# Kernel optimization log

Measured on AMD Instinct MI355X. Metric: run time of the kernel, lower is better.

## Reference

```python
import jax, jax.numpy as jnp
import numpy as np

N_NODES = 100000
N_EDGES = 1600000
N_GRAPHS = 256
NODE_F = 92
EDGE_F = 41
HID = 64


def setup_inputs() -> dict:
    key = jax.random.key(0)
    ks = jax.random.split(key, 16)
    Z = 2 * HID + EDGE_F  # 169, concat dim for CGConv
    inp = {
        "x": jax.random.normal(ks[0], (N_NODES, NODE_F), dtype=jnp.float32),
        "edge_index": jax.random.randint(ks[1], (2, N_EDGES), 0, N_NODES, dtype=jnp.int64),
        "edge_attr": jax.random.uniform(ks[2], (N_EDGES, EDGE_F), dtype=jnp.float32),
        "batch": jnp.sort(jax.random.randint(ks[3], (N_NODES,), 0, N_GRAPHS, dtype=jnp.int64)),
        # embedding Linear(node_feat_dim -> hidden)
        "emb_W": jax.random.normal(ks[4], (NODE_F, HID), dtype=jnp.float32) / np.sqrt(NODE_F),
        "emb_b": jnp.zeros((HID,), dtype=jnp.float32),
        # CGConv layer 1: gate (sigmoid) and source (softplus) linears on z=[x_i,x_j,e]
        "c1_Wf": jax.random.normal(ks[5], (Z, HID), dtype=jnp.float32) / np.sqrt(Z),
        "c1_bf": jnp.zeros((HID,), dtype=jnp.float32),
        "c1_Ws": jax.random.normal(ks[6], (Z, HID), dtype=jnp.float32) / np.sqrt(Z),
        "c1_bs": jnp.zeros((HID,), dtype=jnp.float32),
        # CGConv layer 2
        "c2_Wf": jax.random.normal(ks[7], (Z, HID), dtype=jnp.float32) / np.sqrt(Z),
        "c2_bf": jnp.zeros((HID,), dtype=jnp.float32),
        "c2_Ws": jax.random.normal(ks[8], (Z, HID), dtype=jnp.float32) / np.sqrt(Z),
        "c2_bs": jnp.zeros((HID,), dtype=jnp.float32),
        # head
        "l1_W": jax.random.normal(ks[9], (HID, 32), dtype=jnp.float32) / np.sqrt(HID),
        "l1_b": jnp.zeros((32,), dtype=jnp.float32),
        "l2_W": jax.random.normal(ks[10], (32, 2), dtype=jnp.float32) / np.sqrt(32),
        "l2_b": jnp.zeros((2,), dtype=jnp.float32),
    }
    return inp


def _cgconv(x, src, dst, edge_attr, Wf, bf, Ws, bs):
    # PyG CGConv: z = [x_i (target), x_j (source), e_ij]; msg = sigmoid(lin_f(z)) * softplus(lin_s(z))
    z = jnp.concatenate([x[dst], x[src], edge_attr], axis=-1)  # [E, 2H+D]
    msg = jax.nn.sigmoid(z @ Wf + bf) * jax.nn.softplus(z @ Ws + bs)  # [E, H]
    agg = jax.ops.segment_sum(msg, dst, num_segments=x.shape[0])  # scatter-add at targets
    return x + agg  # residual


def reference(x, edge_index, edge_attr, batch,
              emb_W, emb_b, c1_Wf, c1_bf, c1_Ws, c1_bs,
              c2_Wf, c2_bf, c2_Ws, c2_bs, l1_W, l1_b, l2_W, l2_b):
    src = edge_index[0]  # x_j
    dst = edge_index[1]  # x_i
    h = jax.nn.relu(x @ emb_W + emb_b)
    h = jax.nn.relu(_cgconv(h, src, dst, edge_attr, c1_Wf, c1_bf, c1_Ws, c1_bs))
    h = jax.nn.relu(_cgconv(h, src, dst, edge_attr, c2_Wf, c2_bf, c2_Ws, c2_bs))
    # global_mean_pool over graph ids
    sums = jax.ops.segment_sum(h, batch, num_segments=N_GRAPHS)
    cnt = jax.ops.segment_sum(jnp.ones((h.shape[0],), h.dtype), batch, num_segments=N_GRAPHS)
    pooled = sums / jnp.maximum(cnt, 1.0)[:, None]
    g = jax.nn.relu(pooled @ l1_W + l1_b)
    return g @ l2_W + l2_b  # [N_GRAPHS, 2]
```

## Files before the change

kernel.cpp:

```cpp
#include <hip/hip_runtime.h>

#define N_NODES 100000
#define N_EDGES 1600000
#define N_GRAPHS 256
#define NODE_F 92
#define EDGE_F 41
#define HID 64

typedef float f2 __attribute__((ext_vector_type(2)));
typedef float f4 __attribute__((ext_vector_type(4)));

static __device__ __forceinline__ f2 pk_fma(f2 a, f2 b, f2 c) {
    return __builtin_elementwise_fma(a, b, c);
}

__global__ __launch_bounds__(256) void k_embed(const float* __restrict__ x,
                                               const float* __restrict__ W,
                                               const float* __restrict__ b,
                                               float* __restrict__ h) {
    __shared__ float sT[23 * 256];
    for (int i = threadIdx.x; i < 23 * 256; i += 256) {
        const int kq = i >> 8, rem = i & 255, ln = rem >> 2, kk = rem & 3;
        sT[i] = W[(4 * kq + kk) * HID + ln];
    }
    __syncthreads();
    const int lane = threadIdx.x & 63;
    const int wid  = threadIdx.x >> 6;
    const int nW   = gridDim.x * 4;
    const float bias = b[lane];
    for (int n = blockIdx.x * 4 + wid; n < N_NODES; n += nW) {
        const float* xr = x + (size_t)n * NODE_F;
        float acc = bias;
#pragma unroll
        for (int k0 = 0; k0 < NODE_F; k0 += 4) {
            const f4 xv = *(const f4*)&xr[k0];
            const f4 wv = *(const f4*)&sT[(k0 >> 2) * 256 + 4 * lane];
            acc = fmaf(xv.x, wv.x, acc);
            acc = fmaf(xv.y, wv.y, acc);
            acc = fmaf(xv.z, wv.z, acc);
            acc = fmaf(xv.w, wv.w, acc);
        }
        h[(size_t)n * HID + lane] = fmaxf(acc, 0.f);
    }
}

template <int RELU_IN>
__global__ __launch_bounds__(256) void k_node_pre(const float* hin,
                                                  float* hout,
                                                  const float* __restrict__ Wf,
                                                  const float* __restrict__ Ws,
                                                  float* __restrict__ D,
                                                  float* __restrict__ S) {
    __shared__ float sW[64 * 256];
    for (int i = threadIdx.x; i < 64 * 256; i += 256) {
        const int k = i >> 8, j = i & 255, c = j >> 2, r = j & 3;
        float v;
        if (r == 0)      v = Wf[k * HID + c];
        else if (r == 1) v = Ws[k * HID + c];
        else if (r == 2) v = Wf[(64 + k) * HID + c];
        else             v = Ws[(64 + k) * HID + c];
        sW[i] = v;
    }
    __syncthreads();
    const int lane = threadIdx.x & 63;
    const int wid  = threadIdx.x >> 6;
    const int wave = blockIdx.x * 4 + wid;
    const int nW   = gridDim.x * 4;
    for (int base = wave * 8; base < N_NODES; base += nW * 8) {
        f2 accD[8] = {};
        f2 accS[8] = {};
        for (int k0 = 0; k0 < HID; k0 += 4) {
            f4 wv[4];
#pragma unroll
            for (int kk = 0; kk < 4; ++kk)
                wv[kk] = *(const f4*)&sW[(k0 + kk) * 256 + 4 * lane];
#pragma unroll
            for (int m = 0; m < 8; ++m) {
                f4 hv = *(const f4*)&hin[(size_t)(base + m) * HID + k0];
                if (RELU_IN) {
                    hv.x = fmaxf(hv.x, 0.f); hv.y = fmaxf(hv.y, 0.f);
                    hv.z = fmaxf(hv.z, 0.f); hv.w = fmaxf(hv.w, 0.f);
                }
#pragma unroll
                for (int kk = 0; kk < 4; ++kk) {
                    const f2 ev2 = {hv[kk], hv[kk]};
                    const f2 lo = __builtin_shufflevector(wv[kk], wv[kk], 0, 1);
                    const f2 hi = __builtin_shufflevector(wv[kk], wv[kk], 2, 3);
                    accD[m] = pk_fma(ev2, lo, accD[m]);
                    accS[m] = pk_fma(ev2, hi, accS[m]);
                }
            }
        }
#pragma unroll
        for (int m = 0; m < 8; ++m) {
            const size_t n = base + m;
            *(f2*)&D[n * 128 + 2 * lane] = accD[m];
            *(f2*)&S[n * 128 + 2 * lane] = accS[m];
            if (RELU_IN) hout[n * HID + lane] = fmaxf(hin[n * HID + lane], 0.f);
        }
    }
}

__global__ __launch_bounds__(256) void k_edge(const int* __restrict__ ei,
                                              const float* __restrict__ ea,
                                              const float* __restrict__ D,
                                              const float* __restrict__ S,
                                              const float* __restrict__ Wf,
                                              const float* __restrict__ Ws,
                                              const float* __restrict__ bf,
                                              const float* __restrict__ bs,
                                              float* __restrict__ agg) {
    const int lane = threadIdx.x & 63;
    f2 w[EDGE_F];
#pragma unroll
    for (int k = 0; k < EDGE_F; ++k)
        w[k] = (f2){Wf[(128 + k) * HID + lane], Ws[(128 + k) * HID + lane]};
    const f2 bias = {bf[lane], bs[lane]};
    const int wave = blockIdx.x * 4 + (threadIdx.x >> 6);
    const int nW   = gridDim.x * 4;
    for (int e0 = wave * 2; e0 < N_EDGES; e0 += nW * 2) {
        const int eA = __builtin_amdgcn_readfirstlane(e0);
        const int eB = eA + 1;
        const int srcA = __builtin_amdgcn_readfirstlane(ei[eA]);
        const int dstA = __builtin_amdgcn_readfirstlane(ei[N_EDGES + eA]);
        const int srcB = __builtin_amdgcn_readfirstlane(ei[eB]);
        const int dstB = __builtin_amdgcn_readfirstlane(ei[N_EDGES + eB]);
        const float* erA = ea + (size_t)eA * EDGE_F;
        const float* erB = ea + (size_t)eB * EDGE_F;
        f2 a0 = bias + *(const f2*)&D[(size_t)dstA * 128 + 2 * lane];
        f2 a1 = *(const f2*)&S[(size_t)srcA * 128 + 2 * lane];
        f2 b0 = bias + *(const f2*)&D[(size_t)dstB * 128 + 2 * lane];
        f2 b1 = *(const f2*)&S[(size_t)srcB * 128 + 2 * lane];
#pragma unroll
        for (int k = 0; k + 1 < EDGE_F; k += 2) {
            const float ea0 = erA[k], ea1 = erA[k + 1];
            const float eb0 = erB[k], eb1 = erB[k + 1];
            a0 = pk_fma((f2){ea0, ea0}, w[k], a0);
            b0 = pk_fma((f2){eb0, eb0}, w[k], b0);
            a1 = pk_fma((f2){ea1, ea1}, w[k + 1], a1);
            b1 = pk_fma((f2){eb1, eb1}, w[k + 1], b1);
        }
        {
            const float ea0 = erA[EDGE_F - 1], eb0 = erB[EDGE_F - 1];
            a0 = pk_fma((f2){ea0, ea0}, w[EDGE_F - 1], a0);
            b0 = pk_fma((f2){eb0, eb0}, w[EDGE_F - 1], b0);
        }
        const f2 fsA = a0 + a1;
        const f2 fsB = b0 + b1;
        const float gateA = __builtin_amdgcn_rcpf(1.f + __expf(-fsA.x));
        const float spA   = fmaxf(fsA.y, 0.f) + __logf(1.f + __expf(-fabsf(fsA.y)));
        const float gateB = __builtin_amdgcn_rcpf(1.f + __expf(-fsB.x));
        const float spB   = fmaxf(fsB.y, 0.f) + __logf(1.f + __expf(-fabsf(fsB.y)));
        unsafeAtomicAdd(&agg[(size_t)dstA * HID + lane], gateA * spA);
        unsafeAtomicAdd(&agg[(size_t)dstB * HID + lane], gateB * spB);
    }
}

__global__ __launch_bounds__(256) void k_pool(const float* __restrict__ agg,
                                              const int* __restrict__ batch,
                                              float* __restrict__ psum,
                                              float* __restrict__ pcnt) {
    const int lane = threadIdx.x & 63;
    const int wid  = threadIdx.x >> 6;
    const int wave = blockIdx.x * 4 + wid;
    const int nW   = gridDim.x * 4;
    const int chunk = (N_NODES + nW - 1) / nW;
    const int n0 = wave * chunk;
    if (n0 >= N_NODES) return;
    const int n1 = min(n0 + chunk, N_NODES);
    float acc = 0.f;
    int cur = batch[n0];
    int run = 0;
    for (int n = n0; n < n1; ++n) {
        const int g = batch[n];
        if (g != cur) {
            unsafeAtomicAdd(&psum[(size_t)cur * HID + lane], acc);
            if (lane == 0) unsafeAtomicAdd(&pcnt[cur], (float)run);
            acc = 0.f; run = 0; cur = g;
        }
        acc += fmaxf(agg[(size_t)n * HID + lane], 0.f);
        ++run;
    }
    unsafeAtomicAdd(&psum[(size_t)cur * HID + lane], acc);
    if (lane == 0) unsafeAtomicAdd(&pcnt[cur], (float)run);
}

__global__ __launch_bounds__(256) void k_head(const float* __restrict__ psum,
                                              const float* __restrict__ pcnt,
                                              const float* __restrict__ l1W,
                                              const float* __restrict__ l1b,
                                              const float* __restrict__ l2W,
                                              const float* __restrict__ l2b,
                                              float* __restrict__ out) {
    const int g = threadIdx.x;
    const float inv = 1.f / fmaxf(pcnt[g], 1.f);
    float hid[32];
#pragma unroll
    for (int j = 0; j < 32; ++j) hid[j] = l1b[j];
    for (int c = 0; c < HID; ++c) {
        const float pv = psum[(size_t)g * HID + c] * inv;
#pragma unroll
        for (int j = 0; j < 32; ++j) hid[j] = fmaf(pv, l1W[c * 32 + j], hid[j]);
    }
#pragma unroll
    for (int j = 0; j < 32; ++j) hid[j] = fmaxf(hid[j], 0.f);
#pragma unroll
    for (int k = 0; k < 2; ++k) {
        float a = l2b[k];
#pragma unroll
        for (int j = 0; j < 32; ++j) a = fmaf(hid[j], l2W[j * 2 + k], a);
        out[g * 2 + k] = a;
    }
}

extern "C" void kernel_launch(void* const* d_in, const int* in_sizes, int n_in,
                              void* d_out, int out_size, void* d_ws, size_t ws_size,
                              hipStream_t stream) {
    const float* x     = (const float*)d_in[0];
    const int*   ei    = (const int*)d_in[1];
    const float* ea    = (const float*)d_in[2];
    const int*   batch = (const int*)d_in[3];
    const float* embW  = (const float*)d_in[4];
    const float* embb  = (const float*)d_in[5];
    const float* c1Wf  = (const float*)d_in[6];
    const float* c1bf  = (const float*)d_in[7];
    const float* c1Ws  = (const float*)d_in[8];
    const float* c1bs  = (const float*)d_in[9];
    const float* c2Wf  = (const float*)d_in[10];
    const float* c2bf  = (const float*)d_in[11];
    const float* c2Ws  = (const float*)d_in[12];
    const float* c2bs  = (const float*)d_in[13];
    const float* l1W   = (const float*)d_in[14];
    const float* l1b   = (const float*)d_in[15];
    const float* l2W   = (const float*)d_in[16];
    const float* l2b   = (const float*)d_in[17];
    float* out = (float*)d_out;

    char* w = (char*)d_ws;
    float* A    = (float*)w; w += (size_t)N_NODES * HID * sizeof(float);
    float* D    = (float*)w; w += (size_t)N_NODES * 128 * sizeof(float);
    float* S    = (float*)w; w += (size_t)N_NODES * 128 * sizeof(float);
    float* psum = (float*)w; w += (size_t)N_GRAPHS * HID * sizeof(float);
    float* pcnt = (float*)w; w += (size_t)N_GRAPHS * sizeof(float);

    hipMemsetAsync(psum, 0, (size_t)(N_GRAPHS * HID + N_GRAPHS) * sizeof(float), stream);

    k_embed<<<1024, 256, 0, stream>>>(x, embW, embb, A);

    k_node_pre<0><<<1024, 256, 0, stream>>>(A, A, c1Wf, c1Ws, D, S);
    k_edge<<<2048, 256, 0, stream>>>(ei, ea, D, S, c1Wf, c1Ws, c1bf, c1bs, A);

    k_node_pre<1><<<1024, 256, 0, stream>>>(A, A, c2Wf, c2Ws, D, S);
    k_edge<<<2048, 256, 0, stream>>>(ei, ea, D, S, c2Wf, c2Ws, c2bf, c2bs, A);

    k_pool<<<512, 256, 0, stream>>>(A, batch, psum, pcnt);
    k_head<<<1, 256, 0, stream>>>(psum, pcnt, l1W, l1b, l2W, l2b, out);
}
```

Baseline: 1.824 ms.

## Build dst-sorted CSR and replace atomic edge scatter with per-node gather

Adds a per-call CSR build (histogram of destinations, three-stage prefix scan, atomic scatter of src/edge-id pairs) and replaces the edge kernel's per-edge float atomics into agg with a per-destination-node gather. Each wave walks one node's incoming edges, sums the messages in registers and writes the node row once, with the residual folded in. This removes 1.6M×64 atomic adds per layer and reuses the destination's D row across its edges. The cost is extra kernels plus an int atomic pass on every call, random gathers of edge_attr rows by edge id, and load imbalance across nodes with different in-degree. The packed-FMA node_pre is also rewritten to scalar FMAs, and readfirstlane is used for node indices.

```diff
diff --git a/kernel.cpp b/kernel.cpp
--- a/kernel.cpp
+++ b/kernel.cpp
@@ -6,13 +6,10 @@
 #define NODE_F 92
 #define EDGE_F 41
 #define HID 64
+#define NCHUNK 98
 
 typedef float f2 __attribute__((ext_vector_type(2)));
 typedef float f4 __attribute__((ext_vector_type(4)));
-
-static __device__ __forceinline__ f2 pk_fma(f2 a, f2 b, f2 c) {
-    return __builtin_elementwise_fma(a, b, c);
-}
 
 __global__ __launch_bounds__(256) void k_embed(const float* __restrict__ x,
                                                const float* __restrict__ W,
@@ -25,10 +22,10 @@
     }
     __syncthreads();
     const int lane = threadIdx.x & 63;
-    const int wid  = threadIdx.x >> 6;
     const int nW   = gridDim.x * 4;
     const float bias = b[lane];
-    for (int n = blockIdx.x * 4 + wid; n < N_NODES; n += nW) {
+    for (int n0 = blockIdx.x * 4 + (threadIdx.x >> 6); n0 < N_NODES; n0 += nW) {
+        const int n = __builtin_amdgcn_readfirstlane(n0);
         const float* xr = x + (size_t)n * NODE_F;
         float acc = bias;
 #pragma unroll
@@ -41,6 +38,89 @@
             acc = fmaf(xv.w, wv.w, acc);
         }
         h[(size_t)n * HID + lane] = fmaxf(acc, 0.f);
+    }
+}
+
+__global__ __launch_bounds__(256) void k_hist(const int* __restrict__ ei,
+                                              int* __restrict__ cnt) {
+    for (int i = blockIdx.x * 256 + threadIdx.x; i < N_EDGES; i += gridDim.x * 256)
+        atomicAdd(&cnt[ei[N_EDGES + i]], 1);
+}
+
+__global__ __launch_bounds__(256) void k_scan1(const int* __restrict__ cnt,
+                                               int* __restrict__ csum) {
+    __shared__ int red[256];
+    const int b = blockIdx.x, t = threadIdx.x;
+    int s = 0;
+    for (int i = t; i < 1024; i += 256) {
+        const int g = b * 1024 + i;
+        s += (g < N_NODES) ? cnt[g] : 0;
+    }
+    red[t] = s;
+    __syncthreads();
+    for (int off = 128; off > 0; off >>= 1) {
+        if (t < off) red[t] += red[t + off];
+        __syncthreads();
+    }
+    if (t == 0) csum[b] = red[0];
+}
+
+__global__ __launch_bounds__(128) void k_scan2(const int* __restrict__ csum,
+                                               int* __restrict__ cbase) {
+    __shared__ int sh[128];
+    const int t = threadIdx.x;
+    const int v0 = (t < NCHUNK) ? csum[t] : 0;
+    sh[t] = v0;
+    __syncthreads();
+    for (int off = 1; off < 128; off <<= 1) {
+        const int v = (t >= off) ? sh[t - off] : 0;
+        __syncthreads();
+        sh[t] += v;
+        __syncthreads();
+    }
+    if (t < NCHUNK) cbase[t] = sh[t] - v0;
+}
+
+__global__ __launch_bounds__(256) void k_scan3(const int* __restrict__ cnt,
+                                               const int* __restrict__ cbase,
+                                               int* __restrict__ offs,
+                                               int* __restrict__ woffs) {
+    __shared__ int sh[256];
+    const int b = blockIdx.x, t = threadIdx.x;
+    const int g0 = b * 1024 + t * 4;
+    int v[4], s = 0;
+#pragma unroll
+    for (int k = 0; k < 4; ++k) {
+        const int g = g0 + k;
+        v[k] = (g < N_NODES) ? cnt[g] : 0;
+        s += v[k];
+    }
+    sh[t] = s;
+    __syncthreads();
+    for (int off = 1; off < 256; off <<= 1) {
+        const int x = (t >= off) ? sh[t - off] : 0;
+        __syncthreads();
+        sh[t] += x;
+        __syncthreads();
+    }
+    int base = cbase[b] + sh[t] - s;
+#pragma unroll
+    for (int k = 0; k < 4; ++k) {
+        const int g = g0 + k;
+        if (g < N_NODES) { offs[g] = base; woffs[g] = base; }
+        base += v[k];
+    }
+    if (b == 0 && t == 0) offs[N_NODES] = N_EDGES;
+}
+
+__global__ __launch_bounds__(256) void k_scatter(const int* __restrict__ ei,
+                                                 int* __restrict__ woffs,
+                                                 int2* __restrict__ csr) {
+    for (int i = blockIdx.x * 256 + threadIdx.x; i < N_EDGES; i += gridDim.x * 256) {
+        const int src = ei[i];
+        const int dst = ei[N_EDGES + i];
+        const int pos = atomicAdd(&woffs[dst], 1);
+        csr[pos] = make_int2(src, i);
     }
 }
 
@@ -63,12 +143,11 @@
     }
     __syncthreads();
     const int lane = threadIdx.x & 63;
-    const int wid  = threadIdx.x >> 6;
-    const int wave = blockIdx.x * 4 + wid;
+    const int wave = blockIdx.x * 4 + (threadIdx.x >> 6);
     const int nW   = gridDim.x * 4;
-    for (int base = wave * 8; base < N_NODES; base += nW * 8) {
-        f2 accD[8] = {};
-        f2 accS[8] = {};
+    for (int base0 = wave * 8; base0 < N_NODES; base0 += nW * 8) {
+        const int base = __builtin_amdgcn_readfirstlane(base0);
+        float aD0[8] = {}, aD1[8] = {}, aS0[8] = {}, aS1[8] = {};
         for (int k0 = 0; k0 < HID; k0 += 4) {
             f4 wv[4];
 #pragma unroll
@@ -83,76 +162,92 @@
                 }
 #pragma unroll
                 for (int kk = 0; kk < 4; ++kk) {
-                    const f2 ev2 = {hv[kk], hv[kk]};
-                    const f2 lo = __builtin_shufflevector(wv[kk], wv[kk], 0, 1);
-                    const f2 hi = __builtin_shufflevector(wv[kk], wv[kk], 2, 3);
-                    accD[m] = pk_fma(ev2, lo, accD[m]);
-                    accS[m] = pk_fma(ev2, hi, accS[m]);
+                    aD0[m] = fmaf(hv[kk], wv[kk].x, aD0[m]);
+                    aD1[m] = fmaf(hv[kk], wv[kk].y, aD1[m]);
+                    aS0[m] = fmaf(hv[kk], wv[kk].z, aS0[m]);
+                    aS1[m] = fmaf(hv[kk], wv[kk].w, aS1[m]);
                 }
             }
         }
 #pragma unroll
         for (int m = 0; m < 8; ++m) {
             const size_t n = base + m;
-            *(f2*)&D[n * 128 + 2 * lane] = accD[m];
-            *(f2*)&S[n * 128 + 2 * lane] = accS[m];
+            *(f2*)&D[n * 128 + 2 * lane] = (f2){aD0[m], aD1[m]};
+            *(f2*)&S[n * 128 + 2 * lane] = (f2){aS0[m], aS1[m]};
             if (RELU_IN) hout[n * HID + lane] = fmaxf(hin[n * HID + lane], 0.f);
         }
     }
 }
 
-__global__ __launch_bounds__(256) void k_edge(const int* __restrict__ ei,
-                                              const float* __restrict__ ea,
-                                              const float* __restrict__ D,
-                                              const float* __restrict__ S,
-                                              const float* __restrict__ Wf,
-                                              const float* __restrict__ Ws,
-                                              const float* __restrict__ bf,
-                                              const float* __restrict__ bs,
-                                              float* __restrict__ agg) {
+__device__ __forceinline__ float act(float f, float s) {
+    const float gate = __builtin_amdgcn_rcpf(1.f + __expf(-f));
+    const float sp   = fmaxf(s, 0.f) + __logf(1.f + __expf(-fabsf(s)));
+    return gate * sp;
+}
+
+__global__ __launch_bounds__(256, 4) void k_gather(const int2* __restrict__ csr,
+                                                   const int* __restrict__ offs,
+                                                   const float* __restrict__ ea,
+                                                   const float* __restrict__ D,
+                                                   const float* __restrict__ S,
+                                                   const float* __restrict__ Wf,
+                                                   const float* __restrict__ Ws,
+                                                   const float* __restrict__ bf,
+                                                   const float* __restrict__ bs,
+                                                   const float* hres,
+                                                   float* agg) {
     const int lane = threadIdx.x & 63;
-    f2 w[EDGE_F];
-#pragma unroll
-    for (int k = 0; k < EDGE_F; ++k)
-        w[k] = (f2){Wf[(128 + k) * HID + lane], Ws[(128 + k) * HID + lane]};
-    const f2 bias = {bf[lane], bs[lane]};
-    const int wave = blockIdx.x * 4 + (threadIdx.x >> 6);
-    const int nW   = gridDim.x * 4;
-    for (int e0 = wave * 2; e0 < N_EDGES; e0 += nW * 2) {
-        const int eA = __builtin_amdgcn_readfirstlane(e0);
-        const int eB = eA + 1;
-        const int srcA = __builtin_amdgcn_readfirstlane(ei[eA]);
-        const int dstA = __builtin_amdgcn_readfirstlane(ei[N_EDGES + eA]);
-        const int srcB = __builtin_amdgcn_readfirstlane(ei[eB]);
-        const int dstB = __builtin_amdgcn_readfirstlane(ei[N_EDGES + eB]);
-        const float* erA = ea + (size_t)eA * EDGE_F;
-        const float* erB = ea + (size_t)eB * EDGE_F;
-        f2 a0 = bias + *(const f2*)&D[(size_t)dstA * 128 + 2 * lane];
-        f2 a1 = *(const f2*)&S[(size_t)srcA * 128 + 2 * lane];
-        f2 b0 = bias + *(const f2*)&D[(size_t)dstB * 128 + 2 * lane];
-        f2 b1 = *(const f2*)&S[(size_t)srcB * 128 + 2 * lane];
-#pragma unroll
-        for (int k = 0; k + 1 < EDGE_F; k += 2) {
-            const float ea0 = erA[k], ea1 = erA[k + 1];
-            const float eb0 = erB[k], eb1 = erB[k + 1];
-            a0 = pk_fma((f2){ea0, ea0}, w[k], a0);
-            b0 = pk_fma((f2){eb0, eb0}, w[k], b0);
-            a1 = pk_fma((f2){ea1, ea1}, w[k + 1], a1);
-            b1 = pk_fma((f2){eb1, eb1}, w[k + 1], b1);
-        }
-        {
-            const float ea0 = erA[EDGE_F - 1], eb0 = erB[EDGE_F - 1];
-            a0 = pk_fma((f2){ea0, ea0}, w[EDGE_F - 1], a0);
-            b0 = pk_fma((f2){eb0, eb0}, w[EDGE_F - 1], b0);
-        }
-        const f2 fsA = a0 + a1;
-        const f2 fsB = b0 + b1;
-        const float gateA = __builtin_amdgcn_rcpf(1.f + __expf(-fsA.x));
-        const float spA   = fmaxf(fsA.y, 0.f) + __logf(1.f + __expf(-fabsf(fsA.y)));
-        const float gateB = __builtin_amdgcn_rcpf(1.f + __expf(-fsB.x));
-        const float spB   = fmaxf(fsB.y, 0.f) + __logf(1.f + __expf(-fabsf(fsB.y)));
-        unsafeAtomicAdd(&agg[(size_t)dstA * HID + lane], gateA * spA);
-        unsafeAtomicAdd(&agg[(size_t)dstB * HID + lane], gateB * spB);
+    float wf[EDGE_F], ws[EDGE_F];
+#pragma unroll
+    for (int k = 0; k < EDGE_F; ++k) {
+        wf[k] = Wf[(128 + k) * HID + lane];
+        ws[k] = Ws[(128 + k) * HID + lane];
+    }
+    const float bfv = bf[lane], bsv = bs[lane];
+    const int nW = gridDim.x * 4;
+    for (int n0 = blockIdx.x * 4 + (threadIdx.x >> 6); n0 < N_NODES; n0 += nW) {
+        const int n  = __builtin_amdgcn_readfirstlane(n0);
+        const int j0 = offs[n];
+        const int j1 = offs[n + 1];
+        float acc = hres[(size_t)n * HID + lane];
+        const f2 dv = *(const f2*)&D[(size_t)n * 128 + 2 * lane];
+        const float bD0 = bfv + dv.x, bD1 = bsv + dv.y;
+        int j = j0;
+        for (; j + 1 < j1; j += 2) {
+            const int2 c0 = csr[j], c1 = csr[j + 1];
+            const int s0 = __builtin_amdgcn_readfirstlane(c0.x);
+            const int e0 = __builtin_amdgcn_readfirstlane(c0.y);
+            const int s1 = __builtin_amdgcn_readfirstlane(c1.x);
+            const int e1 = __builtin_amdgcn_readfirstlane(c1.y);
+            const f2 sv0 = *(const f2*)&S[(size_t)s0 * 128 + 2 * lane];
+            const f2 sv1 = *(const f2*)&S[(size_t)s1 * 128 + 2 * lane];
+            const float* r0 = ea + (size_t)e0 * EDGE_F;
+            const float* r1 = ea + (size_t)e1 * EDGE_F;
+            float f0 = bD0 + sv0.x, q0 = bD1 + sv0.y;
+            float f1 = bD0 + sv1.x, q1 = bD1 + sv1.y;
+#pragma unroll
+            for (int k = 0; k < EDGE_F; ++k) {
+                const float a = r0[k], b = r1[k];
+                f0 = fmaf(a, wf[k], f0); q0 = fmaf(a, ws[k], q0);
+                f1 = fmaf(b, wf[k], f1); q1 = fmaf(b, ws[k], q1);
+            }
+            acc += act(f0, q0) + act(f1, q1);
+        }
+        if (j < j1) {
+            const int2 c0 = csr[j];
+            const int s0 = __builtin_amdgcn_readfirstlane(c0.x);
+            const int e0 = __builtin_amdgcn_readfirstlane(c0.y);
+            const f2 sv0 = *(const f2*)&S[(size_t)s0 * 128 + 2 * lane];
+            const float* r0 = ea + (size_t)e0 * EDGE_F;
+            float f0 = bD0 + sv0.x, q0 = bD1 + sv0.y;
+#pragma unroll
+            for (int k = 0; k < EDGE_F; ++k) {
+                const float a = r0[k];
+                f0 = fmaf(a, wf[k], f0); q0 = fmaf(a, ws[k], q0);
+            }
+            acc += act(f0, q0);
+        }
+        agg[(size_t)n * HID + lane] = acc;
     }
 }
 
@@ -161,8 +256,7 @@
                                               float* __restrict__ psum,
                                               float* __restrict__ pcnt) {
     const int lane = threadIdx.x & 63;
-    const int wid  = threadIdx.x >> 6;
-    const int wave = blockIdx.x * 4 + wid;
+    const int wave = blockIdx.x * 4 + (threadIdx.x >> 6);
     const int nW   = gridDim.x * 4;
     const int chunk = (N_NODES + nW - 1) / nW;
     const int n0 = wave * chunk;
@@ -240,18 +334,30 @@
     float* A    = (float*)w; w += (size_t)N_NODES * HID * sizeof(float);
     float* D    = (float*)w; w += (size_t)N_NODES * 128 * sizeof(float);
     float* S    = (float*)w; w += (size_t)N_NODES * 128 * sizeof(float);
+    int2*  csr  = (int2*)w;  w += (size_t)N_EDGES * sizeof(int2);
+    int*   cnt  = (int*)w;   w += (size_t)((N_NODES + 4) & ~3) * sizeof(int);
+    int*   offs = (int*)w;   w += (size_t)((N_NODES + 4) & ~3) * sizeof(int);
+    int*   woffs= (int*)w;   w += (size_t)((N_NODES + 4) & ~3) * sizeof(int);
+    int*   csum = (int*)w;   w += 128 * sizeof(int);
+    int*   cbase= (int*)w;   w += 128 * sizeof(int);
     float* psum = (float*)w; w += (size_t)N_GRAPHS * HID * sizeof(float);
     float* pcnt = (float*)w; w += (size_t)N_GRAPHS * sizeof(float);
 
+    hipMemsetAsync(cnt, 0, (size_t)N_NODES * sizeof(int), stream);
     hipMemsetAsync(psum, 0, (size_t)(N_GRAPHS * HID + N_GRAPHS) * sizeof(float), stream);
 
     k_embed<<<1024, 256, 0, stream>>>(x, embW, embb, A);
+    k_hist<<<1024, 256, 0, stream>>>(ei, cnt);
+    k_scan1<<<NCHUNK, 256, 0, stream>>>(cnt, csum);
+    k_scan2<<<1, 128, 0, stream>>>(csum, cbase);
+    k_scan3<<<NCHUNK, 256, 0, stream>>>(cnt, cbase, offs, woffs);
+    k_scatter<<<1024, 256, 0, stream>>>(ei, woffs, csr);
 
     k_node_pre<0><<<1024, 256, 0, stream>>>(A, A, c1Wf, c1Ws, D, S);
-    k_edge<<<2048, 256, 0, stream>>>(ei, ea, D, S, c1Wf, c1Ws, c1bf, c1bs, A);
+    k_gather<<<2048, 256, 0, stream>>>(csr, offs, ea, D, S, c1Wf, c1Ws, c1bf, c1bs, A, A);
 
     k_node_pre<1><<<1024, 256, 0, stream>>>(A, A, c2Wf, c2Ws, D, S);
-    k_edge<<<2048, 256, 0, stream>>>(ei, ea, D, S, c2Wf, c2Ws, c2bf, c2bs, A);
+    k_gather<<<2048, 256, 0, stream>>>(csr, offs, ea, D, S, c2Wf, c2Ws, c2bf, c2bs, A, A);
 
     k_pool<<<512, 256, 0, stream>>>(A, batch, psum, pcnt);
     k_head<<<1, 256, 0, stream>>>(psum, pcnt, l1W, l1b, l2W, l2b, out);
```

Measured after the change: 1.944 ms. +6.6%, slower.
